# Performance work log

Hardware: AMD Instinct MI355X
Metric: run time of the kernel (lower is better)

## Reference

```python
import jax, jax.numpy as jnp
import numpy as np

N = 10000; G = 100; NPG = 100; E = 400000; EPG = 4000
C = 32; L = 3; LM = 16; S = 4; NB = 8; NL = 3
CUT = 6.0; AVG = 40.0
L_OF = np.array([0, 1, 1, 1, 2, 2, 2, 2, 2, 3, 3, 3, 3, 3, 3, 3])  # l of each lm slot


def sph_harm(v):
    # component-normalized real spherical harmonics up to l=3 on unit vectors
    x, y, z = v[..., 0], v[..., 1], v[..., 2]
    s3 = jnp.sqrt(3.0); s5 = jnp.sqrt(5.0); s15 = jnp.sqrt(15.0)
    Y = [jnp.ones_like(x),
         s3 * x, s3 * y, s3 * z,
         s15 * x * y, s15 * y * z, 0.5 * s5 * (3 * z * z - 1.0), s15 * x * z, 0.5 * s15 * (x * x - y * y),
         jnp.sqrt(35.0 / 8.0) * y * (3 * x * x - y * y), jnp.sqrt(105.0) * x * y * z,
         jnp.sqrt(21.0 / 8.0) * y * (5 * z * z - 1.0), 0.5 * jnp.sqrt(7.0) * (5 * z ** 3 - 3 * z),
         jnp.sqrt(21.0 / 8.0) * x * (5 * z * z - 1.0), 0.5 * jnp.sqrt(105.0) * z * (x * x - y * y),
         jnp.sqrt(35.0 / 8.0) * x * (x * x - 3 * y * y)]
    return jnp.stack(Y, axis=-1)  # [E, 16]


def bessel_cutoff(r):
    # bessel basis (r_max=1) * polynomial cutoff (p=2)
    n = jnp.arange(1, NB + 1, dtype=r.dtype)
    rs = jnp.where(r > 1e-9, r, 1e-9)
    b = jnp.sqrt(2.0) * jnp.sin(jnp.pi * n[None, :] * rs[:, None]) / rs[:, None]
    f = jnp.where(r < 1.0, 1.0 - 6.0 * r ** 2 + 8.0 * r ** 3 - 3.0 * r ** 4, 0.0)
    return b * f[:, None]  # [E, NB]


def setup_inputs() -> dict:
    key = jax.random.key(0)
    ks = jax.random.split(key, 20)
    positions = jax.random.normal(ks[0], (N, 3), dtype=jnp.float32)
    cell = jnp.eye(3, dtype=jnp.float32)[None] * 3.0 + 0.05 * jax.random.normal(ks[1], (G, 3, 3), dtype=jnp.float32)
    Sij = jax.random.randint(ks[2], (E, 3), 0, 3).astype(jnp.int32) - 1
    gid = jnp.arange(E, dtype=jnp.int32) // EPG
    ia = gid * NPG + jax.random.randint(ks[3], (E,), 0, NPG).astype(jnp.int32)
    ja = gid * NPG + jax.random.randint(ks[4], (E,), 0, NPG).astype(jnp.int32)
    edge_index = jnp.stack([ia, ja], axis=0)
    species = jax.random.randint(ks[5], (N,), 0, S).astype(jnp.int32)
    batch = (jnp.arange(N, dtype=jnp.int32) // NPG)
    sc = 0.1
    return {
        'positions': positions, 'cell': cell, 'Sij': Sij, 'edge_index': edge_index,
        'species': species, 'batch': batch,
        'W_emb': sc * jax.random.normal(ks[6], (S, C), dtype=jnp.float32),
        'W_xtp': sc * jax.random.normal(ks[7], (C, S), dtype=jnp.float32),
        'W_up': sc * jax.random.normal(ks[8], (NL, L + 1, C, C), dtype=jnp.float32),
        'W1': sc * jax.random.normal(ks[9], (NL, NB, 64), dtype=jnp.float32),
        'b1': jnp.zeros((NL, 64), dtype=jnp.float32),
        'W2': sc * jax.random.normal(ks[10], (NL, 64, 64), dtype=jnp.float32),
        'b2': jnp.zeros((NL, 64), dtype=jnp.float32),
        'W3': sc * jax.random.normal(ks[11], (NL, 64, 2 * C * (L + 1)), dtype=jnp.float32),
        'W_down': sc * jax.random.normal(ks[12], (NL, L + 1, C, C), dtype=jnp.float32),
        'W_sc': sc * jax.random.normal(ks[13], (NL, L + 1, C, S, C), dtype=jnp.float32),
        'Wr1': sc * jax.random.normal(ks[14], (NL, C, 64), dtype=jnp.float32),
        'br1': jnp.zeros((NL, 64), dtype=jnp.float32),
        'Wr2': sc * jax.random.normal(ks[15], (NL, 64, 1), dtype=jnp.float32),
    }


def reference(positions, cell, Sij, edge_index, species, batch, W_emb, W_xtp, W_up,
              W1, b1, W2, b2, W3, W_down, W_sc, Wr1, br1, Wr2):
    ia, ja = edge_index[0], edge_index[1]
    eg = batch[ia]  # graph id of each edge
    shift = jnp.einsum('ei,eij->ej', Sij.astype(positions.dtype), cell[eg])
    Rij = (positions[ja] - positions[ia] + shift) / CUT
    r = jnp.linalg.norm(Rij, axis=1)
    u = Rij / jnp.where(r > 1e-9, r, 1e-9)[:, None]
    Y = sph_harm(u)                      # [E, 16]
    ef = bessel_cutoff(r)                # [E, 8]
    attrs = jax.nn.one_hot(species, S, dtype=positions.dtype)
    h0 = attrs @ W_emb                   # node embedding [N, C]
    h = jnp.zeros((N, C, LM), positions.dtype).at[:, :, 0].set(h0)
    xnode = jnp.einsum('nc,ns,cs->n', h0, attrs, W_xtp)  # x_node_tp -> 1x0e
    lof = jnp.asarray(L_OF)
    outs = []
    for layer in range(NL):
        hu = jnp.einsum('ncm,mcd->ndm', h, W_up[layer][lof])  # linear up (per-l)
        hm = jax.nn.silu(ef @ W1[layer] + b1[layer])
        hm = jax.nn.silu(hm @ W2[layer] + b2[layer])
        rw = (hm @ W3[layer]).reshape(-1, 2, C, L + 1)        # per-edge TP weights
        w = rw[:, :, :, lof]                                  # [E, 2, C, 16]
        hj = hu[ja]                                           # gather sender feats
        m = w[:, 0] * Y[:, None, :] * hj[:, :, :1] + w[:, 1] * hj  # depthwise TP paths
        agg = jax.ops.segment_sum(m, ia, num_segments=N) / AVG
        hmsg = jnp.einsum('ncm,mcd->ndm', agg, W_down[layer][lof])
        sc = jnp.einsum('ncm,ns,mcsd->ndm', h, attrs, W_sc[layer][lof])  # self-conn TP
        h = hmsg * xnode[:, None, None] + sc                  # product block
        e = jax.nn.silu(h[:, :, 0] @ Wr1[layer] + br1[layer]) @ Wr2[layer]
        outs.append(e[:, 0])
    node_e = jax.nn.silu(jnp.stack(outs, -1)).sum(-1)
    return jax.ops.segment_sum(node_e, batch, num_segments=G)  # per-graph energy [G]
```

## Files before the change

kernel.cpp:

```cpp
#include <hip/hip_runtime.h>
#include <hip/hip_bf16.h>
#include <hip/hip_fp16.h>
#include <stdint.h>

#define NN   10000
#define GG   100
#define NPG  100
#define EE   400000
#define EPG  4000
#define CC   32
#define LM   16
#define SS   4
#define NBES 8
#define NLAYER 3
#define INV_AVG (1.0f/40.0f)
#define MLPB 6256

typedef _Float16 f16x8 __attribute__((ext_vector_type(8)));
typedef _Float16 f16x4 __attribute__((ext_vector_type(4)));
typedef _Float16 f16x2 __attribute__((ext_vector_type(2)));
typedef float    f32x4 __attribute__((ext_vector_type(4)));

__device__ __forceinline__ float siluf(float x) { return x / (1.0f + __expf(-x)); }
__device__ __forceinline__ int lof(int m) { return (m >= 1) + (m >= 4) + (m >= 9); }
__device__ __forceinline__ f16x2 asf16x2(unsigned u) {
  union { unsigned u; f16x2 f; } x; x.u = u; return x.f;
}

__device__ __forceinline__ void gload_lds16(const void* g, void* l) {
  __builtin_amdgcn_global_load_lds(
      (const __attribute__((address_space(1))) unsigned int*)g,
      (__attribute__((address_space(3))) unsigned int*)l, 16, 0, 0);
}

__device__ __forceinline__ void geom_body(
    int e, const float* __restrict__ pos, const float* __restrict__ cell,
    const int* __restrict__ Sij, const int* __restrict__ eidx,
    const int* __restrict__ batch, __half* __restrict__ Y, __half* __restrict__ ef)
{
  int ia = eidx[e], ja = eidx[EE + e];
  int g = batch[ia];
  float s0 = (float)Sij[e*3+0], s1 = (float)Sij[e*3+1], s2 = (float)Sij[e*3+2];
  const float* cg = cell + g*9;
  float shx = s0*cg[0] + s1*cg[3] + s2*cg[6];
  float shy = s0*cg[1] + s1*cg[4] + s2*cg[7];
  float shz = s0*cg[2] + s1*cg[5] + s2*cg[8];
  float rx = (pos[ja*3+0] - pos[ia*3+0] + shx) / 6.0f;
  float ry = (pos[ja*3+1] - pos[ia*3+1] + shy) / 6.0f;
  float rz = (pos[ja*3+2] - pos[ia*3+2] + shz) / 6.0f;
  float r2 = rx*rx + ry*ry + rz*rz;
  float r  = sqrtf(r2);
  float rs = (r > 1e-9f) ? r : 1e-9f;
  float inv = 1.0f / rs;
  float x = rx*inv, y = ry*inv, z = rz*inv;

  const float s3   = 1.7320508075688772f;
  const float s15  = 3.872983346207417f;
  const float s5h  = 1.118033988749895f;
  const float s15h = 1.9364916731037085f;
  const float s358 = 2.091650066335189f;
  const float s105 = 10.246950765959598f;
  const float s218 = 1.620185174601965f;
  const float s7h  = 1.3228756555322954f;
  const float s105h= 5.123475382979799f;

  float xx = x*x, yy = y*y, zz = z*z;
  float yv[16];
  yv[0]  = 1.0f;
  yv[1]  = s3*x;  yv[2] = s3*y;  yv[3] = s3*z;
  yv[4]  = s15*x*y; yv[5] = s15*y*z; yv[6] = s5h*(3.0f*zz - 1.0f);
  yv[7]  = s15*x*z; yv[8] = s15h*(xx - yy);
  yv[9]  = s358*y*(3.0f*xx - yy);
  yv[10] = s105*x*y*z;
  yv[11] = s218*y*(5.0f*zz - 1.0f);
  yv[12] = s7h*(5.0f*zz*z - 3.0f*z);
  yv[13] = s218*x*(5.0f*zz - 1.0f);
  yv[14] = s105h*z*(xx - yy);
  yv[15] = s358*x*(xx - 3.0f*yy);

  union { __half h[16]; uint4 u[2]; } yp;
  #pragma unroll
  for (int i = 0; i < 16; ++i) yp.h[i] = __float2half(yv[i]);
  uint4* Yp = (uint4*)(Y + (size_t)e*16);
  Yp[0] = yp.u[0];
  Yp[1] = yp.u[1];

  float f = 0.0f;
  if (r < 1.0f) f = 1.0f - 6.0f*r2 + 8.0f*r2*r - 3.0f*r2*r2;
  float c1 = 1.4142135623730951f * f * inv;
  float ang = 3.14159265358979323846f * rs;
  float sn = __sinf(ang), cn = __cosf(ang);
  float twoc = 2.0f * cn;
  float sprev = 0.0f, scur = sn;
  union { __half h[8]; uint4 u; } p;
  #pragma unroll
  for (int n1 = 1; n1 <= NBES; ++n1) {
    p.h[n1-1] = __float2half(c1 * scur);
    float snext = twoc * scur - sprev;
    sprev = scur; scur = snext;
  }
  *(uint4*)(ef + (size_t)e*8) = p.u;
}

__global__ __launch_bounds__(256) void k_pre(
    const float* __restrict__ pos, const float* __restrict__ cell,
    const int* __restrict__ Sij, const int* __restrict__ eidx,
    const int* __restrict__ batch, __half* __restrict__ Y, __half* __restrict__ ef,
    const int* __restrict__ species, const float* __restrict__ W_emb,
    const float* __restrict__ W_xtp, float* __restrict__ h,
    float* __restrict__ xnode, float* __restrict__ node_e,
    const float* __restrict__ W2, const float* __restrict__ W3,
    _Float16* __restrict__ W2t, _Float16* __restrict__ W3t,
    const float* __restrict__ W_up0, float* __restrict__ hu0,
    int* __restrict__ cnt)
{
  int b = blockIdx.x, t = threadIdx.x;
  if (b < 1563) {
    int e = b*256 + t;
    if (e < EE) geom_body(e, pos, cell, Sij, eidx, batch, Y, ef);
  } else if (b < 2813) {
    int idx = (b - 1563)*256 + t;
    if (idx < NN*CC) {
      int n = idx / CC, c = idx % CC;
      int sp = species[n];
      float h0 = W_emb[sp*CC + c];
      float* hp = h + (size_t)n*512 + c*16;
      hp[0] = h0;
      #pragma unroll
      for (int m = 1; m < 16; ++m) hp[m] = 0.0f;
      if (c == 0) {
        float xn = 0.0f;
        for (int c2 = 0; c2 < CC; ++c2) xn += W_emb[sp*CC + c2] * W_xtp[c2*SS + sp];
        xnode[n] = xn;
        node_e[n] = 0.0f;
      }
    }
  } else if (b < 3005) {
    int idx = (b - 2813)*256 + t;
    if (idx < NLAYER*64*64) {
      int l = idx / 4096, rem = idx % 4096, k = rem / 64, j = rem % 64;
      W2t[l*4096 + j*64 + k] = (_Float16)W2[idx];
    }
    if (idx < NLAYER*64*256) {
      int l = idx / 16384, rem = idx % 16384, k = rem / 256, j = rem % 256;
      W3t[l*16384 + j*64 + k] = (_Float16)W3[idx];
    }
    if (b == 2813 && idx < SS*CC) {
      int sp = idx >> 5, dd = idx & 31;
      float p0 = 0.0f, p1 = 0.0f;
      for (int c2 = 0; c2 < 16; ++c2)  p0 += W_emb[sp*CC + c2] * W_up0[c2*32 + dd];
      for (int c2 = 16; c2 < 32; ++c2) p1 += W_emb[sp*CC + c2] * W_up0[c2*32 + dd];
      hu0[idx] = p0 + p1;
    }
  } else {
    int e = (b - 3005)*256 + t;
    if (e < EE) atomicAdd(&cnt[eidx[e]], 1);
  }
}

__global__ __launch_bounds__(128) void k_csr_scan(
    const int* __restrict__ cnt, int* __restrict__ off, int* __restrict__ cursor) {
  __shared__ int s[128];
  int g = blockIdx.x, t = threadIdx.x;
  int own = (t < NPG) ? cnt[g*NPG + t] : 0;
  s[t] = own;
  __syncthreads();
  #pragma unroll
  for (int d = 1; d < 128; d <<= 1) {
    int v = (t >= d) ? s[t-d] : 0;
    __syncthreads();
    s[t] += v;
    __syncthreads();
  }
  if (t < NPG) {
    int o = g*EPG + s[t] - own;
    off[g*NPG + t] = o;
    cursor[g*NPG + t] = o;
    if (g == GG-1 && t == NPG-1) off[NN] = EE;
  }
}

__device__ __forceinline__ void mlp_body(
    int mb, int t, _Float16* pool16,
    const __half* __restrict__ ef, const float* __restrict__ W1,
    const float* __restrict__ b1, const _Float16* __restrict__ W2t,
    const float* __restrict__ b2, __half* __restrict__ hm2)
{
  int eb = (mb & 7) * 782 + (mb >> 3);
  if (eb >= EE/64) return;
  int wv = t >> 6, lane = t & 63;
  int ln15 = lane & 15, quad = lane >> 4;
  _Float16* hm1 = pool16 + wv*(16*72);
  size_t e16 = (size_t)eb*64 + wv*16;

  union { uint4 u; __half hh[8]; } efv;
  efv.u = *(const uint4*)(ef + (e16 + ln15)*8);
  float ev[8];
  #pragma unroll
  for (int k = 0; k < 8; ++k) ev[k] = __half2float(efv.hh[k]);
  #pragma unroll
  for (int p = 0; p < 4; ++p) {
    int j0 = p*16 + quad*4;
    float4 a = *(const float4*)(b1 + j0);
    #pragma unroll
    for (int k = 0; k < 8; ++k) {
      const float4 w = *(const float4*)(W1 + k*64 + j0);
      a.x += ev[k]*w.x; a.y += ev[k]*w.y; a.z += ev[k]*w.z; a.w += ev[k]*w.w;
    }
    f16x4 pk;
    pk[0] = (_Float16)siluf(a.x);
    pk[1] = (_Float16)siluf(a.y);
    pk[2] = (_Float16)siluf(a.z);
    pk[3] = (_Float16)siluf(a.w);
    *(f16x4*)&hm1[ln15*72 + j0] = pk;
  }

  f16x8 a0 = *(const f16x8*)(hm1 + ln15*72 + quad*8);
  f16x8 a1 = *(const f16x8*)(hm1 + ln15*72 + 32 + quad*8);
  #pragma unroll
  for (int cg = 0; cg < 4; ++cg) {
    int col = cg*16 + ln15;
    f32x4 d = {0.f, 0.f, 0.f, 0.f};
    d = __builtin_amdgcn_mfma_f32_16x16x32_f16(a0, *(const f16x8*)(W2t + (size_t)col*64 + quad*8), d, 0, 0, 0);
    d = __builtin_amdgcn_mfma_f32_16x16x32_f16(a1, *(const f16x8*)(W2t + (size_t)col*64 + 32 + quad*8), d, 0, 0, 0);
    float bb = b2[col];
    #pragma unroll
    for (int r = 0; r < 4; ++r)
      hm2[(e16 + quad*4 + r)*64 + col] = __float2half(siluf(d[r] + bb));
  }
}

__global__ __launch_bounds__(256) void k_mlp(
    const __half* __restrict__ ef, const float* __restrict__ W1,
    const float* __restrict__ b1, const _Float16* __restrict__ W2t,
    const float* __restrict__ b2, __half* __restrict__ hm2)
{
  __shared__ _Float16 pool16[4*16*72];
  mlp_body(blockIdx.x, threadIdx.x, pool16, ef, W1, b1, W2t, b2, hm2);
}

__global__ __launch_bounds__(256) void k_csr_fill(
    const int* __restrict__ eidx, int* __restrict__ cursor, int2* __restrict__ elist,
    const float* __restrict__ hu0, const int* __restrict__ species,
    __half* __restrict__ huA,
    const __half* __restrict__ ef, const float* __restrict__ W1,
    const float* __restrict__ b1, const _Float16* __restrict__ W2t,
    const float* __restrict__ b2, __half* __restrict__ hm2) {
  __shared__ _Float16 pool16[4*16*72];
  int b = blockIdx.x;
  if (b < 1563) {
    int e = b * 256 + threadIdx.x;
    if (e >= EE) return;
    int ia = eidx[e], ja = eidx[EE + e];
    int pos = atomicAdd(&cursor[ia], 1);
    elist[pos] = make_int2(e*128, ja*1024);
    return;
  }
  if (b < 2813) {
    int idx = (b - 1563)*256 + threadIdx.x;
    if (idx >= NN*CC) return;
    int n = idx >> 5, d = idx & 31;
    __half h0 = __float2half(hu0[species[n]*CC + d]);
    union { __half hh[2]; unsigned u; } w; w.hh[0] = h0; w.hh[1] = __half(0.0f);
    uint4 v0 = make_uint4(w.u, 0u, 0u, 0u);
    uint4 v1 = make_uint4(0u, 0u, 0u, 0u);
    uint4* p = (uint4*)(huA + (size_t)n*512 + d*16);
    p[0] = v0;
    p[1] = v1;
    return;
  }
  mlp_body(b - 2813, threadIdx.x, pool16, ef, W1, b1, W2t, b2, hm2);
}

__global__ __launch_bounds__(256) void k_gather(
    const int2* __restrict__ elist, const int* __restrict__ off,
    const __half* __restrict__ Y, const __half* __restrict__ hm2,
    const _Float16* __restrict__ W3t, const __half* __restrict__ hu_in,
    const int* __restrict__ species, const float* __restrict__ xnode,
    const float* __restrict__ Wd, const float* __restrict__ Wsc,
    const float* __restrict__ Wr1, const float* __restrict__ br1,
    const float* __restrict__ Wr2, float* __restrict__ node_e,
    const float* __restrict__ Wu_next, __half* __restrict__ hu_out,
    float* __restrict__ h, int has_next,
    int do_mlp, const __half* __restrict__ ef,
    const float* __restrict__ W1n, const float* __restrict__ b1n,
    const _Float16* __restrict__ W2tn, const float* __restrict__ b2n,
    __half* __restrict__ hm2_next)
{
  __shared__ float pool[6656];

  int b = blockIdx.x, t = threadIdx.x;
  if (do_mlp) {
    if (b < MLPB) {
      mlp_body(b, t, (_Float16*)pool, ef, W1n, b1n, W2tn, b2n, hm2_next);
      return;
    }
    b -= MLPB;
  }
  _Float16* rw_base = (_Float16*)pool;
  char* hu_sc = (char*)pool + 8704;
  char* Ys_c  = (char*)pool + 25600;
  float* al_s = pool;
  float* h2_s = pool + 512;

  int n = (b & 7) * (NN/8) + (b >> 3);
  int beg = off[n], deg = off[n+1] - beg;

  int lane = t & 63, wv = t >> 6;
  int ln15 = lane & 15, quad = lane >> 4;
  _Float16* rww = rw_base + wv*(16*68);
  const char* rwc = (const char*)rww;
  const char* hm2c = (const char*)hm2;
  const char* Yc   = (const char*)Y;
  const char* huc  = (const char*)hu_in;

  float hreg0 = h[(size_t)n*512 + t];
  float hreg1 = h[(size_t)n*512 + t + 256];

  int mq   = lane & 3;
  int cl   = (lane >> 2) & 7;
  int half = lane >> 5;
  int c    = wv*8 + cl;
  int m0q  = mq*4;
  int la0 = lof(m0q),   lb0 = lof(m0q+1);
  int la1 = lof(m0q+2), lb1 = lof(m0q+3);
  unsigned sel0 = (unsigned)(2*la0) | ((unsigned)(2*la0+1)<<8)
                | ((unsigned)(2*lb0)<<16) | ((unsigned)(2*lb0+1)<<24);
  unsigned sel1 = (unsigned)(2*la1) | ((unsigned)(2*la1+1)<<8)
                | ((unsigned)(2*lb1)<<16) | ((unsigned)(2*lb1+1)<<24);
  unsigned huconst = (unsigned)(c*32 + mq*8);

  f16x8 w3A[4], w3B[4];
  #pragma unroll
  for (int cg = 0; cg < 4; ++cg) {
    int colg = (cg < 2) ? (wv*32 + cg*16 + ln15)
                        : (128 + wv*32 + (cg-2)*16 + ln15);
    w3A[cg] = *(const f16x8*)(W3t + (size_t)colg*64 + quad*8);
    w3B[cg] = *(const f16x8*)(W3t + (size_t)colg*64 + 32 + quad*8);
  }

  float acc0 = 0.f, acc1 = 0.f, acc2 = 0.f, acc3 = 0.f;

  int2 el_cur = make_int2(0, 0);
  f16x8 aA0 = {}, aA1 = {};
  if (deg > 0) {
    int idx = lane < deg ? lane : deg - 1;
    el_cur = elist[beg + idx];
    int eA = __shfl(el_cur.x, ln15);
    aA0 = *(const f16x8*)(hm2c + (unsigned)eA + quad*16);
    aA1 = *(const f16x8*)(hm2c + (unsigned)eA + 64 + quad*16);
  }

  auto edge_compute = [&](int s, f16x2& av0, f16x2& av1) {
    uint2 hj = *(const uint2*)(hu_sc + (unsigned)s*1056 + huconst);
    unsigned hj0b = (unsigned)__builtin_amdgcn_mov_dpp((int)hj.x, 0, 0xf, 0xf, true);
    unsigned hj0s = __builtin_amdgcn_perm(hj0b, hj0b, 0x01000100u);
    uint2 Ymv = *(const uint2*)(Ys_c + (unsigned)s*32 + mq*8);
    uint2 w0q = *(const uint2*)(rwc + (unsigned)s*136 + cl*8);
    uint2 w1q = *(const uint2*)(rwc + (unsigned)s*136 + cl*8 + 64);
    unsigned w00 = __builtin_amdgcn_perm(w0q.y, w0q.x, sel0);
    unsigned w01 = __builtin_amdgcn_perm(w0q.y, w0q.x, sel1);
    unsigned w10 = __builtin_amdgcn_perm(w1q.y, w1q.x, sel0);
    unsigned w11 = __builtin_amdgcn_perm(w1q.y, w1q.x, sel1);
    f16x2 hj0v = asf16x2(hj0s);
    av0 += asf16x2(w00) * (asf16x2(Ymv.x) * hj0v) + asf16x2(w10) * asf16x2(hj.x);
    av1 += asf16x2(w01) * (asf16x2(Ymv.y) * hj0v) + asf16x2(w11) * asf16x2(hj.y);
  };

  for (int base = 0; base < deg; base += 16) {
    int cnt = deg - base; if (cnt > 16) cnt = 16;

    if (base > 0) __syncthreads();

    #pragma unroll
    for (int q = 0; q < 4; ++q) {
      int s = wv*4 + q;
      if (s < cnt) {
        int rowoff = __shfl(el_cur.y, s);
        gload_lds16(huc + (unsigned)rowoff + lane*16, hu_sc + s*1056);
      }
    }
    if (wv == 0) {
      int yoff = __shfl(el_cur.x, lane >> 1) >> 2;
      gload_lds16(Yc + (unsigned)yoff + (lane & 1)*16, Ys_c);
    }

    __builtin_amdgcn_s_setprio(1);
    #pragma unroll
    for (int cg = 0; cg < 4; ++cg) {
      f32x4 dA = {0.f, 0.f, 0.f, 0.f};
      dA = __builtin_amdgcn_mfma_f32_16x16x32_f16(w3A[cg], aA0, dA, 0, 0, 0);
      dA = __builtin_amdgcn_mfma_f32_16x16x32_f16(w3B[cg], aA1, dA, 0, 0, 0);
      f16x4 pA;
      #pragma unroll
      for (int r = 0; r < 4; ++r) pA[r] = (_Float16)dA[r];
      *(f16x4*)&rww[ln15*68 + cg*16 + quad*4] = pA;
    }
    __builtin_amdgcn_s_setprio(0);

    __syncthreads();

    int2 el_nxt = el_cur;
    f16x8 nA0 = aA0, nA1 = aA1;
    if (base + 16 < deg) {
      int idx = base + 16 + lane;
      if (idx >= deg) idx = deg - 1;
      el_nxt = elist[beg + idx];
      int eA = __shfl(el_nxt.x, ln15);
      nA0 = *(const f16x8*)(hm2c + (unsigned)eA + quad*16);
      nA1 = *(const f16x8*)(hm2c + (unsigned)eA + 64 + quad*16);
    }

    f16x2 av0 = {(_Float16)0.f, (_Float16)0.f};
    f16x2 av1 = {(_Float16)0.f, (_Float16)0.f};
    int nfull = cnt >> 1;
    #pragma unroll 8
    for (int i = 0; i < nfull; ++i) edge_compute(2*i + half, av0, av1);
    if ((cnt & 1) && half == 0) edge_compute(cnt - 1, av0, av1);
    acc0 += (float)av0[0]; acc1 += (float)av0[1];
    acc2 += (float)av1[0]; acc3 += (float)av1[1];

    el_cur = el_nxt;
    aA0 = nA0; aA1 = nA1;
  }

  acc0 += __shfl_xor(acc0, 32);
  acc1 += __shfl_xor(acc1, 32);
  acc2 += __shfl_xor(acc2, 32);
  acc3 += __shfl_xor(acc3, 32);

  __syncthreads();

  if (half == 0) {
    *(float4*)&al_s[c*16 + m0q] =
        make_float4(acc0*INV_AVG, acc1*INV_AVG, acc2*INV_AVG, acc3*INV_AVG);
  }
  h2_s[t]       = hreg0;
  h2_s[t + 256] = hreg1;
  __syncthreads();

  int sp = species[n];
  float xn = xnode[n];
  int d = lane & 31, ch = lane >> 5;
  #pragma unroll
  for (int mi = 0; mi < 4; ++mi) {
    int m = wv*4 + mi;
    int l = lof(m);
    const float* wd  = Wd  + l*1024 + d;
    const float* wsc = Wsc + l*4096 + sp*32 + d;
    float a = 0.0f, s = 0.0f;
    #pragma unroll 4
    for (int cc = 0; cc < 16; ++cc) {
      int c2 = cc + ch*16;
      a += al_s[c2*16 + m] * wd[c2*32];
      s += h2_s[c2*16 + m] * wsc[c2*128];
    }
    a += __shfl_xor(a, 32);
    s += __shfl_xor(s, 32);
    float hn = a*xn + s;
    if (ch == 0) h2_s[d*16 + m] = hn;
    if (has_next) {
      const float* wu = Wu_next + l*1024 + d;
      float u = 0.0f;
      #pragma unroll 4
      for (int cc = 0; cc < 16; ++cc) {
        int c2 = cc + ch*16;
        u += h2_s[c2*16 + m] * wu[c2*32];
      }
      u += __shfl_xor(u, 32);
      if (ch == 0) al_s[d*16 + m] = u;
    }
  }

  if (t < 64) {
    float pre = br1[t];
    #pragma unroll 4
    for (int cc = 0; cc < CC; ++cc) pre += h2_s[cc*16] * Wr1[cc*64 + t];
    float v = siluf(pre) * Wr2[t];
    #pragma unroll
    for (int off2 = 32; off2 > 0; off2 >>= 1) v += __shfl_down(v, off2);
    if (t == 0) node_e[n] += siluf(v);
  }
  __syncthreads();

  h[(size_t)n*512 + t]       = h2_s[t];
  h[(size_t)n*512 + t + 256] = h2_s[t + 256];
  if (has_next) {
    __half2 o;
    o.x = __float2half(al_s[2*t]);
    o.y = __float2half(al_s[2*t + 1]);
    *(__half2*)(hu_out + (size_t)n*512 + 2*t) = o;
  }
}

__global__ __launch_bounds__(128) void k_out(
    const float* __restrict__ node_e, float* __restrict__ out)
{
  int g = blockIdx.x, t = threadIdx.x;
  float v = (t < NPG) ? node_e[g*NPG + t] : 0.0f;
  #pragma unroll
  for (int off2 = 32; off2 > 0; off2 >>= 1) v += __shfl_down(v, off2);
  __shared__ float r2[2];
  if ((t & 63) == 0) r2[t >> 6] = v;
  __syncthreads();
  if (t == 0) out[g] = r2[0] + r2[1];
}

__global__ void k_dbg(float* __restrict__ out, float v) {
  int i = blockIdx.x * 64 + threadIdx.x;
  if (i < GG) out[i] = v;
}

extern "C" void kernel_launch(void* const* d_in, const int* in_sizes, int n_in,
                              void* d_out, int out_size, void* d_ws, size_t ws_size,
                              hipStream_t stream)
{
  const float* positions = (const float*)d_in[0];
  const float* cell      = (const float*)d_in[1];
  const int*   Sij       = (const int*)d_in[2];
  const int*   eidx      = (const int*)d_in[3];
  const int*   species   = (const int*)d_in[4];
  const int*   batch     = (const int*)d_in[5];
  const float* W_emb     = (const float*)d_in[6];
  const float* W_xtp     = (const float*)d_in[7];
  const float* W_up      = (const float*)d_in[8];
  const float* W1        = (const float*)d_in[9];
  const float* b1        = (const float*)d_in[10];
  const float* W2        = (const float*)d_in[11];
  const float* b2        = (const float*)d_in[12];
  const float* W3        = (const float*)d_in[13];
  const float* W_down    = (const float*)d_in[14];
  const float* W_sc      = (const float*)d_in[15];
  const float* Wr1       = (const float*)d_in[16];
  const float* br1       = (const float*)d_in[17];
  const float* Wr2       = (const float*)d_in[18];
  float* out = (float*)d_out;
  (void)in_sizes; (void)n_in; (void)out_size;

  const size_t NEED_BASE  = 120000000;
  const size_t NEED_FUSED = 166500000;
  if (ws_size < NEED_BASE) {
    k_dbg<<<dim3(2), dim3(64), 0, stream>>>(out, (float)(ws_size >> 20));
    return;
  }
  const bool fused = ws_size >= NEED_FUSED;

  char* ws = (char*)d_ws;
  size_t off = 0;
  auto alloc = [&](size_t bytes) -> void* {
    void* p = ws + off;
    off += (bytes + 255) & ~(size_t)255;
    return p;
  };
  __half*    Yb      = (__half*)alloc((size_t)EE*16*2);
  __half*    efb     = (__half*)alloc((size_t)EE*8*2);
  float*     hb      = (float*)alloc((size_t)NN*512*4);
  __half*    huA     = (__half*)alloc((size_t)NN*512*2);
  __half*    huB     = (__half*)alloc((size_t)NN*512*2);
  float*     xnodeb  = (float*)alloc((size_t)NN*4);
  float*     node_eb = (float*)alloc((size_t)NN*4);
  int*       offb    = (int*)alloc((size_t)(NN+1)*4);
  int*       curb    = (int*)alloc((size_t)NN*4);
  int2*      elistb  = (int2*)alloc((size_t)EE*8);
  _Float16*  W2tb    = (_Float16*)alloc((size_t)NLAYER*64*64*2);
  _Float16*  W3tb    = (_Float16*)alloc((size_t)NLAYER*64*256*2);
  float*     hu0b    = (float*)alloc((size_t)SS*CC*4);
  __half*    hm2A    = (__half*)alloc((size_t)EE*64*2);
  __half*    hm2B    = fused ? (__half*)alloc((size_t)EE*64*2) : hm2A;

  dim3 blk(256);
  hipMemsetAsync(curb, 0, (size_t)NN*4, stream);
  k_pre<<<dim3(4568), blk, 0, stream>>>(positions, cell, Sij, eidx, batch,
      Yb, efb, species, W_emb, W_xtp, hb, xnodeb, node_eb,
      W2, W3, W2tb, W3tb, W_up, hu0b, curb);
  k_csr_scan<<<dim3(GG), dim3(128), 0, stream>>>(curb, offb, curb);
  k_csr_fill<<<dim3(2813 + MLPB), blk, 0, stream>>>(eidx, curb, elistb,
      hu0b, species, huA,
      efb, W1 + 0, b1 + 0, W2tb + 0, b2 + 0, hm2A);

  __half* hin = huA; __half* hout = huB;
  __half* hm2_cur = hm2A; __half* hm2_nxt = hm2B;
  for (int layer = 0; layer < NLAYER; ++layer) {
    int has_next = (layer + 1 < NLAYER) ? 1 : 0;
    int do_mlp = (fused && has_next) ? 1 : 0;
    int nl = has_next ? layer + 1 : 0;
    k_gather<<<dim3(NN + (do_mlp ? MLPB : 0)), blk, 0, stream>>>(
        elistb, offb, Yb, hm2_cur,
        W3tb + layer*16384, hin,
        species, xnodeb,
        W_down + layer*4096, W_sc + layer*16384,
        Wr1 + layer*CC*64, br1 + layer*64, Wr2 + layer*64, node_eb,
        W_up + (has_next ? (layer+1)*4096 : 0), hout, hb, has_next,
        do_mlp, efb,
        W1 + nl*NBES*64, b1 + nl*64, W2tb + nl*4096, b2 + nl*64,
        hm2_nxt);
    if (!fused && has_next) {
      k_mlp<<<dim3(MLPB), blk, 0, stream>>>(efb,
          W1 + (layer+1)*NBES*64, b1 + (layer+1)*64,
          W2tb + (layer+1)*4096, b2 + (layer+1)*64, hm2A);
    }
    __half* tmp = hin; hin = hout; hout = tmp;
    if (fused) { __half* t2 = hm2_cur; hm2_cur = hm2_nxt; hm2_nxt = t2; }
  }
  k_out<<<dim3(GG), dim3(128), 0, stream>>>(node_eb, out);
}
```

Baseline: 819.0 us.

## Pack two nodes per 512-thread block in gather kernel

Widens k_gather to 512-thread blocks, with each 256-thread half processing its own node (and, in the fused MLP part, its own MLP tile) in a separate shared-memory region. Both halves iterate to the larger of the two degree tile counts and skip work when inactive, so the block-wide barriers stay consistent. The goal is to halve the block count and cut per-block launch and scheduling overhead. In exchange, shared memory per block doubles, the half holding the lower-degree node idles at barriers, and the higher register cap under 512-thread launch bounds may reduce occupancy.

```diff
diff --git a/kernel.cpp b/kernel.cpp
--- a/kernel.cpp
+++ b/kernel.cpp
@@ -15,6 +15,7 @@
 #define NLAYER 3
 #define INV_AVG (1.0f/40.0f)
 #define MLPB 6256
+#define MLPB2 3128
 
 typedef _Float16 f16x8 __attribute__((ext_vector_type(8)));
 typedef _Float16 f16x4 __attribute__((ext_vector_type(4)));
@@ -272,7 +273,7 @@
   mlp_body(b - 2813, threadIdx.x, pool16, ef, W1, b1, W2t, b2, hm2);
 }
 
-__global__ __launch_bounds__(256) void k_gather(
+__global__ __launch_bounds__(512) void k_gather(
     const int2* __restrict__ elist, const int* __restrict__ off,
     const __half* __restrict__ Y, const __half* __restrict__ hm2,
     const _Float16* __restrict__ W3t, const __half* __restrict__ hu_in,
@@ -287,26 +288,31 @@
     const _Float16* __restrict__ W2tn, const float* __restrict__ b2n,
     __half* __restrict__ hm2_next)
 {
-  __shared__ float pool[6656];
+  __shared__ float pool[13312];
+  __shared__ int nt2[2];
 
   int b = blockIdx.x, t = threadIdx.x;
+  int unit = t >> 8, tt = t & 255;
   if (do_mlp) {
-    if (b < MLPB) {
-      mlp_body(b, t, (_Float16*)pool, ef, W1n, b1n, W2tn, b2n, hm2_next);
+    if (b < MLPB2) {
+      mlp_body(b*2 + unit, tt, (_Float16*)pool + unit*4608,
+               ef, W1n, b1n, W2tn, b2n, hm2_next);
       return;
     }
-    b -= MLPB;
-  }
-  _Float16* rw_base = (_Float16*)pool;
-  char* hu_sc = (char*)pool + 8704;
-  char* Ys_c  = (char*)pool + 25600;
-  float* al_s = pool;
-  float* h2_s = pool + 512;
-
-  int n = (b & 7) * (NN/8) + (b >> 3);
+    b -= MLPB2;
+  }
+  float* upool = pool + unit*6656;
+  _Float16* rw_base = (_Float16*)upool;
+  char* hu_sc = (char*)upool + 8704;
+  char* Ys_c  = (char*)upool + 25600;
+  float* al_s = upool;
+  float* h2_s = upool + 512;
+
+  int u = b*2 + unit;
+  int n = (u & 7) * (NN/8) + (u >> 3);
   int beg = off[n], deg = off[n+1] - beg;
 
-  int lane = t & 63, wv = t >> 6;
+  int lane = tt & 63, wv = tt >> 6;
   int ln15 = lane & 15, quad = lane >> 4;
   _Float16* rww = rw_base + wv*(16*68);
   const char* rwc = (const char*)rww;
@@ -314,8 +320,8 @@
   const char* Yc   = (const char*)Y;
   const char* huc  = (const char*)hu_in;
 
-  float hreg0 = h[(size_t)n*512 + t];
-  float hreg1 = h[(size_t)n*512 + t + 256];
+  float hreg0 = h[(size_t)n*512 + tt];
+  float hreg1 = h[(size_t)n*512 + tt + 256];
 
   int mq   = lane & 3;
   int cl   = (lane >> 2) & 7;
@@ -338,6 +344,10 @@
     w3A[cg] = *(const f16x8*)(W3t + (size_t)colg*64 + quad*8);
     w3B[cg] = *(const f16x8*)(W3t + (size_t)colg*64 + 32 + quad*8);
   }
+
+  if (tt == 0) nt2[unit] = (deg + 15) >> 4;
+  __syncthreads();
+  int ntmax = max(nt2[0], nt2[1]);
 
   float acc0 = 0.f, acc1 = 0.f, acc2 = 0.f, acc3 = 0.f;
 
@@ -367,61 +377,68 @@
     av1 += asf16x2(w01) * (asf16x2(Ymv.y) * hj0v) + asf16x2(w11) * asf16x2(hj.y);
   };
 
-  for (int base = 0; base < deg; base += 16) {
-    int cnt = deg - base; if (cnt > 16) cnt = 16;
-
-    if (base > 0) __syncthreads();
-
-    #pragma unroll
-    for (int q = 0; q < 4; ++q) {
-      int s = wv*4 + q;
-      if (s < cnt) {
-        int rowoff = __shfl(el_cur.y, s);
-        gload_lds16(huc + (unsigned)rowoff + lane*16, hu_sc + s*1056);
+  for (int tc = 0; tc < ntmax; ++tc) {
+    int base = tc*16;
+    bool active = base < deg;
+    int cnt = 0;
+    if (active) { cnt = deg - base; if (cnt > 16) cnt = 16; }
+
+    if (tc > 0) __syncthreads();
+
+    if (active) {
+      #pragma unroll
+      for (int q = 0; q < 4; ++q) {
+        int s = wv*4 + q;
+        if (s < cnt) {
+          int rowoff = __shfl(el_cur.y, s);
+          gload_lds16(huc + (unsigned)rowoff + lane*16, hu_sc + s*1056);
+        }
       }
-    }
-    if (wv == 0) {
-      int yoff = __shfl(el_cur.x, lane >> 1) >> 2;
-      gload_lds16(Yc + (unsigned)yoff + (lane & 1)*16, Ys_c);
-    }
-
-    __builtin_amdgcn_s_setprio(1);
-    #pragma unroll
-    for (int cg = 0; cg < 4; ++cg) {
-      f32x4 dA = {0.f, 0.f, 0.f, 0.f};
-      dA = __builtin_amdgcn_mfma_f32_16x16x32_f16(w3A[cg], aA0, dA, 0, 0, 0);
-      dA = __builtin_amdgcn_mfma_f32_16x16x32_f16(w3B[cg], aA1, dA, 0, 0, 0);
-      f16x4 pA;
+      if (wv == 0) {
+        int yoff = __shfl(el_cur.x, lane >> 1) >> 2;
+        gload_lds16(Yc + (unsigned)yoff + (lane & 1)*16, Ys_c);
+      }
+
+      __builtin_amdgcn_s_setprio(1);
       #pragma unroll
-      for (int r = 0; r < 4; ++r) pA[r] = (_Float16)dA[r];
-      *(f16x4*)&rww[ln15*68 + cg*16 + quad*4] = pA;
-    }
-    __builtin_amdgcn_s_setprio(0);
+      for (int cg = 0; cg < 4; ++cg) {
+        f32x4 dA = {0.f, 0.f, 0.f, 0.f};
+        dA = __builtin_amdgcn_mfma_f32_16x16x32_f16(w3A[cg], aA0, dA, 0, 0, 0);
+        dA = __builtin_amdgcn_mfma_f32_16x16x32_f16(w3B[cg], aA1, dA, 0, 0, 0);
+        f16x4 pA;
+        #pragma unroll
+        for (int r = 0; r < 4; ++r) pA[r] = (_Float16)dA[r];
+        *(f16x4*)&rww[ln15*68 + cg*16 + quad*4] = pA;
+      }
+      __builtin_amdgcn_s_setprio(0);
+    }
 
     __syncthreads();
 
-    int2 el_nxt = el_cur;
-    f16x8 nA0 = aA0, nA1 = aA1;
-    if (base + 16 < deg) {
-      int idx = base + 16 + lane;
-      if (idx >= deg) idx = deg - 1;
-      el_nxt = elist[beg + idx];
-      int eA = __shfl(el_nxt.x, ln15);
-      nA0 = *(const f16x8*)(hm2c + (unsigned)eA + quad*16);
-      nA1 = *(const f16x8*)(hm2c + (unsigned)eA + 64 + quad*16);
-    }
-
-    f16x2 av0 = {(_Float16)0.f, (_Float16)0.f};
-    f16x2 av1 = {(_Float16)0.f, (_Float16)0.f};
-    int nfull = cnt >> 1;
-    #pragma unroll 8
-    for (int i = 0; i < nfull; ++i) edge_compute(2*i + half, av0, av1);
-    if ((cnt & 1) && half == 0) edge_compute(cnt - 1, av0, av1);
-    acc0 += (float)av0[0]; acc1 += (float)av0[1];
-    acc2 += (float)av1[0]; acc3 += (float)av1[1];
-
-    el_cur = el_nxt;
-    aA0 = nA0; aA1 = nA1;
+    if (active) {
+      int2 el_nxt = el_cur;
+      f16x8 nA0 = aA0, nA1 = aA1;
+      if (base + 16 < deg) {
+        int idx = base + 16 + lane;
+        if (idx >= deg) idx = deg - 1;
+        el_nxt = elist[beg + idx];
+        int eA = __shfl(el_nxt.x, ln15);
+        nA0 = *(const f16x8*)(hm2c + (unsigned)eA + quad*16);
+        nA1 = *(const f16x8*)(hm2c + (unsigned)eA + 64 + quad*16);
+      }
+
+      f16x2 av0 = {(_Float16)0.f, (_Float16)0.f};
+      f16x2 av1 = {(_Float16)0.f, (_Float16)0.f};
+      int nfull = cnt >> 1;
+      #pragma unroll 8
+      for (int i = 0; i < nfull; ++i) edge_compute(2*i + half, av0, av1);
+      if ((cnt & 1) && half == 0) edge_compute(cnt - 1, av0, av1);
+      acc0 += (float)av0[0]; acc1 += (float)av0[1];
+      acc2 += (float)av1[0]; acc3 += (float)av1[1];
+
+      el_cur = el_nxt;
+      aA0 = nA0; aA1 = nA1;
+    }
   }
 
   acc0 += __shfl_xor(acc0, 32);
@@ -435,8 +452,8 @@
     *(float4*)&al_s[c*16 + m0q] =
         make_float4(acc0*INV_AVG, acc1*INV_AVG, acc2*INV_AVG, acc3*INV_AVG);
   }
-  h2_s[t]       = hreg0;
-  h2_s[t + 256] = hreg1;
+  h2_s[tt]       = hreg0;
+  h2_s[tt + 256] = hreg1;
   __syncthreads();
 
   int sp = species[n];
@@ -461,35 +478,35 @@
     if (ch == 0) h2_s[d*16 + m] = hn;
     if (has_next) {
       const float* wu = Wu_next + l*1024 + d;
-      float u = 0.0f;
+      float uacc = 0.0f;
       #pragma unroll 4
       for (int cc = 0; cc < 16; ++cc) {
         int c2 = cc + ch*16;
-        u += h2_s[c2*16 + m] * wu[c2*32];
+        uacc += h2_s[c2*16 + m] * wu[c2*32];
       }
-      u += __shfl_xor(u, 32);
-      if (ch == 0) al_s[d*16 + m] = u;
-    }
-  }
-
-  if (t < 64) {
-    float pre = br1[t];
+      uacc += __shfl_xor(uacc, 32);
+      if (ch == 0) al_s[d*16 + m] = uacc;
+    }
+  }
+
+  if (tt < 64) {
+    float pre = br1[tt];
     #pragma unroll 4
-    for (int cc = 0; cc < CC; ++cc) pre += h2_s[cc*16] * Wr1[cc*64 + t];
-    float v = siluf(pre) * Wr2[t];
+    for (int cc = 0; cc < CC; ++cc) pre += h2_s[cc*16] * Wr1[cc*64 + tt];
+    float v = siluf(pre) * Wr2[tt];
     #pragma unroll
     for (int off2 = 32; off2 > 0; off2 >>= 1) v += __shfl_down(v, off2);
-    if (t == 0) node_e[n] += siluf(v);
+    if (tt == 0) node_e[n] += siluf(v);
   }
   __syncthreads();
 
-  h[(size_t)n*512 + t]       = h2_s[t];
-  h[(size_t)n*512 + t + 256] = h2_s[t + 256];
+  h[(size_t)n*512 + tt]       = h2_s[tt];
+  h[(size_t)n*512 + tt + 256] = h2_s[tt + 256];
   if (has_next) {
     __half2 o;
-    o.x = __float2half(al_s[2*t]);
-    o.y = __float2half(al_s[2*t + 1]);
-    *(__half2*)(hu_out + (size_t)n*512 + 2*t) = o;
+    o.x = __float2half(al_s[2*tt]);
+    o.y = __float2half(al_s[2*tt + 1]);
+    *(__half2*)(hu_out + (size_t)n*512 + 2*tt) = o;
   }
 }
 
@@ -569,6 +586,7 @@
   __half*    hm2B    = fused ? (__half*)alloc((size_t)EE*64*2) : hm2A;
 
   dim3 blk(256);
+  dim3 blk512(512);
   hipMemsetAsync(curb, 0, (size_t)NN*4, stream);
   k_pre<<<dim3(4568), blk, 0, stream>>>(positions, cell, Sij, eidx, batch,
       Yb, efb, species, W_emb, W_xtp, hb, xnodeb, node_eb,
@@ -584,7 +602,7 @@
     int has_next = (layer + 1 < NLAYER) ? 1 : 0;
     int do_mlp = (fused && has_next) ? 1 : 0;
     int nl = has_next ? layer + 1 : 0;
-    k_gather<<<dim3(NN + (do_mlp ? MLPB : 0)), blk, 0, stream>>>(
+    k_gather<<<dim3(NN/2 + (do_mlp ? MLPB2 : 0)), blk512, 0, stream>>>(
         elistb, offb, Yb, hm2_cur,
         W3tb + layer*16384, hin,
         species, xnodeb,
```

Result: slower. 870.2 us (+6.3%).

## Double-buffer LDS staging of gathered sender features and harmonics across edge chunks

Applied to the files above, without the earlier changes.

The per-node gather loop now keeps two LDS buffers for the gathered sender features and spherical-harmonic rows. The next 16-edge chunk's global-to-LDS loads are issued before the current chunk's MFMA and edge math, and the edge list is prefetched two chunks ahead. This is meant to hide gather latency behind compute and to drop one barrier per chunk. In exchange the shared-memory footprint rises from about 26 KB to about 44 KB. That can lower occupancy, including for the MLP blocks that share this kernel.

```diff
diff --git a/kernel.cpp b/kernel.cpp
--- a/kernel.cpp
+++ b/kernel.cpp
@@ -287,7 +287,7 @@
     const _Float16* __restrict__ W2tn, const float* __restrict__ b2n,
     __half* __restrict__ hm2_next)
 {
-  __shared__ float pool[6656];
+  __shared__ float pool[11136];
 
   int b = blockIdx.x, t = threadIdx.x;
   if (do_mlp) {
@@ -298,8 +298,8 @@
     b -= MLPB;
   }
   _Float16* rw_base = (_Float16*)pool;
-  char* hu_sc = (char*)pool + 8704;
-  char* Ys_c  = (char*)pool + 25600;
+  char* hu_base = (char*)pool + 8704;
+  char* ys_base = (char*)pool + 42496;
   float* al_s = pool;
   float* h2_s = pool + 512;
 
@@ -341,21 +341,38 @@
 
   float acc0 = 0.f, acc1 = 0.f, acc2 = 0.f, acc3 = 0.f;
 
-  int2 el_cur = make_int2(0, 0);
+  int2 el_nx = make_int2(0, 0);
   f16x8 aA0 = {}, aA1 = {};
   if (deg > 0) {
-    int idx = lane < deg ? lane : deg - 1;
-    el_cur = elist[beg + idx];
-    int eA = __shfl(el_cur.x, ln15);
+    int idx0 = lane < deg ? lane : deg - 1;
+    int2 el0 = elist[beg + idx0];
+    int idx1 = 16 + lane; if (idx1 >= deg) idx1 = deg - 1;
+    el_nx = elist[beg + idx1];
+    int eA = __shfl(el0.x, ln15);
     aA0 = *(const f16x8*)(hm2c + (unsigned)eA + quad*16);
     aA1 = *(const f16x8*)(hm2c + (unsigned)eA + 64 + quad*16);
-  }
-
+    int cnt0 = deg < 16 ? deg : 16;
+    #pragma unroll
+    for (int q = 0; q < 4; ++q) {
+      int s = wv*4 + q;
+      if (s < cnt0) {
+        int rowoff = __shfl(el0.y, s);
+        gload_lds16(huc + (unsigned)rowoff + lane*16, hu_base + s*1056);
+      }
+    }
+    if (wv == 0) {
+      int yoff = __shfl(el0.x, lane >> 1) >> 2;
+      gload_lds16(Yc + (unsigned)yoff + (lane & 1)*16, ys_base);
+    }
+  }
+
+  const char* hu_rd = hu_base;
+  const char* ys_rd = ys_base;
   auto edge_compute = [&](int s, f16x2& av0, f16x2& av1) {
-    uint2 hj = *(const uint2*)(hu_sc + (unsigned)s*1056 + huconst);
+    uint2 hj = *(const uint2*)(hu_rd + (unsigned)s*1056 + huconst);
     unsigned hj0b = (unsigned)__builtin_amdgcn_mov_dpp((int)hj.x, 0, 0xf, 0xf, true);
     unsigned hj0s = __builtin_amdgcn_perm(hj0b, hj0b, 0x01000100u);
-    uint2 Ymv = *(const uint2*)(Ys_c + (unsigned)s*32 + mq*8);
+    uint2 Ymv = *(const uint2*)(ys_rd + (unsigned)s*32 + mq*8);
     uint2 w0q = *(const uint2*)(rwc + (unsigned)s*136 + cl*8);
     uint2 w1q = *(const uint2*)(rwc + (unsigned)s*136 + cl*8 + 64);
     unsigned w00 = __builtin_amdgcn_perm(w0q.y, w0q.x, sel0);
@@ -367,22 +384,28 @@
     av1 += asf16x2(w01) * (asf16x2(Ymv.y) * hj0v) + asf16x2(w11) * asf16x2(hj.y);
   };
 
+  int buf = 0;
   for (int base = 0; base < deg; base += 16) {
     int cnt = deg - base; if (cnt > 16) cnt = 16;
 
-    if (base > 0) __syncthreads();
-
-    #pragma unroll
-    for (int q = 0; q < 4; ++q) {
-      int s = wv*4 + q;
-      if (s < cnt) {
-        int rowoff = __shfl(el_cur.y, s);
-        gload_lds16(huc + (unsigned)rowoff + lane*16, hu_sc + s*1056);
+    __syncthreads();
+
+    if (base + 16 < deg) {
+      int cnt1 = deg - base - 16; if (cnt1 > 16) cnt1 = 16;
+      char* hu_wr = hu_base + (buf ^ 1) * 16896;
+      char* ys_wr = ys_base + (buf ^ 1) * 1024;
+      #pragma unroll
+      for (int q = 0; q < 4; ++q) {
+        int s = wv*4 + q;
+        if (s < cnt1) {
+          int rowoff = __shfl(el_nx.y, s);
+          gload_lds16(huc + (unsigned)rowoff + lane*16, hu_wr + s*1056);
+        }
       }
-    }
-    if (wv == 0) {
-      int yoff = __shfl(el_cur.x, lane >> 1) >> 2;
-      gload_lds16(Yc + (unsigned)yoff + (lane & 1)*16, Ys_c);
+      if (wv == 0) {
+        int yoff = __shfl(el_nx.x, lane >> 1) >> 2;
+        gload_lds16(Yc + (unsigned)yoff + (lane & 1)*16, ys_wr);
+      }
     }
 
     __builtin_amdgcn_s_setprio(1);
@@ -398,19 +421,19 @@
     }
     __builtin_amdgcn_s_setprio(0);
 
-    __syncthreads();
-
-    int2 el_nxt = el_cur;
+    int2 el_nn = el_nx;
     f16x8 nA0 = aA0, nA1 = aA1;
     if (base + 16 < deg) {
-      int idx = base + 16 + lane;
+      int idx = base + 32 + lane;
       if (idx >= deg) idx = deg - 1;
-      el_nxt = elist[beg + idx];
-      int eA = __shfl(el_nxt.x, ln15);
+      el_nn = elist[beg + idx];
+      int eA = __shfl(el_nx.x, ln15);
       nA0 = *(const f16x8*)(hm2c + (unsigned)eA + quad*16);
       nA1 = *(const f16x8*)(hm2c + (unsigned)eA + 64 + quad*16);
     }
 
+    hu_rd = hu_base + buf * 16896;
+    ys_rd = ys_base + buf * 1024;
     f16x2 av0 = {(_Float16)0.f, (_Float16)0.f};
     f16x2 av1 = {(_Float16)0.f, (_Float16)0.f};
     int nfull = cnt >> 1;
@@ -420,8 +443,9 @@
     acc0 += (float)av0[0]; acc1 += (float)av0[1];
     acc2 += (float)av1[0]; acc3 += (float)av1[1];
 
-    el_cur = el_nxt;
+    el_nx = el_nn;
     aA0 = nA0; aA1 = nA1;
+    buf ^= 1;
   }
 
   acc0 += __shfl_xor(acc0, 32);
```

New measurement: 907.2 us. +10.8%, slower.
